# Performance work log

Measured on AMD Instinct MI355X. Metric: run time of the kernel, lower is better.

The kernel has to match this reference:

```python
import jax, jax.numpy as jnp
import numpy as np
from jax import lax

B, T, D, LSTM, N_MELS, SPK, NOISE = 256, 600, 256, 512, 80, 256, 64
MAX_R = 10
FC1 = 256
FC2 = D // 2  # 128
FILTERS, KSIZE = 32, 31


def _lin(k, out_d, in_d):
    return jax.random.normal(k, (out_d, in_d), jnp.float32) * 0.02


def setup_inputs() -> dict:
    key = jax.random.key(0)
    ks = list(jax.random.split(key, 40))
    nk = iter(ks)
    inp = {
        "encoder_seq": jax.random.normal(next(nk), (B, T, D), jnp.float32),
        "encoder_seq_proj": jax.random.normal(next(nk), (B, T, D), jnp.float32),
        "prenet_in": jax.random.normal(next(nk), (B, N_MELS), jnp.float32),
        "attn_hidden": jax.random.normal(next(nk), (B, D), jnp.float32),
        "rnn1_hidden": jax.random.normal(next(nk), (B, LSTM), jnp.float32),
        "rnn2_hidden": jax.random.normal(next(nk), (B, LSTM), jnp.float32),
        "rnn1_cell": jax.random.normal(next(nk), (B, LSTM), jnp.float32),
        "rnn2_cell": jax.random.normal(next(nk), (B, LSTM), jnp.float32),
        "context_vec": jax.random.normal(next(nk), (B, D), jnp.float32),
        "speaker_embedding": jax.random.normal(next(nk), (B, SPK), jnp.float32),
        "noise_embedding": jax.random.normal(next(nk), (B, NOISE), jnp.float32),
        "attn_cumulative": jax.random.uniform(next(nk), (B, T), jnp.float32),
        "attn_prev": jax.random.uniform(next(nk), (B, T), jnp.float32),
        "phone_len": jax.random.randint(next(nk), (B,), 1, T + 1),
        # PreNet
        "fc1_w": _lin(next(nk), FC1, N_MELS + NOISE), "fc1_b": jnp.zeros((FC1,), jnp.float32),
        "fc2_w": _lin(next(nk), FC2, FC1), "fc2_b": jnp.zeros((FC2,), jnp.float32),
        # LSA
        "conv_w": jax.random.normal(next(nk), (FILTERS, 2, KSIZE), jnp.float32) * 0.1,
        "L_w": _lin(next(nk), D, FILTERS), "L_b": jnp.zeros((D,), jnp.float32),
        "W_w": _lin(next(nk), D, D), "W_b": jnp.zeros((D,), jnp.float32),
        "v_w": _lin(next(nk), 1, D),
        # attn GRU: input = D + D//2 + SPK
        "gru_wih": _lin(next(nk), 3 * D, D + FC2 + SPK), "gru_whh": _lin(next(nk), 3 * D, D),
        "gru_bih": jnp.zeros((3 * D,), jnp.float32), "gru_bhh": jnp.zeros((3 * D,), jnp.float32),
        # rnn_input Linear: 2*D + SPK + NOISE -> LSTM
        "rnn_in_w": _lin(next(nk), LSTM, 2 * D + SPK + NOISE), "rnn_in_b": jnp.zeros((LSTM,), jnp.float32),
        # two LSTMCells
        "l1_wih": _lin(next(nk), 4 * LSTM, LSTM), "l1_whh": _lin(next(nk), 4 * LSTM, LSTM),
        "l1_bih": jnp.zeros((4 * LSTM,), jnp.float32), "l1_bhh": jnp.zeros((4 * LSTM,), jnp.float32),
        "l2_wih": _lin(next(nk), 4 * LSTM, LSTM), "l2_whh": _lin(next(nk), 4 * LSTM, LSTM),
        "l2_bih": jnp.zeros((4 * LSTM,), jnp.float32), "l2_bhh": jnp.zeros((4 * LSTM,), jnp.float32),
        # mel projection (no bias)
        "mel_w": _lin(next(nk), N_MELS * MAX_R, LSTM),
        "r": 2,
    }
    return inp


def _gru(x, h, wih, whh, bih, bhh):
    gi = x @ wih.T + bih
    gh = h @ whh.T + bhh
    i_r, i_z, i_n = jnp.split(gi, 3, axis=-1)
    h_r, h_z, h_n = jnp.split(gh, 3, axis=-1)
    r = jax.nn.sigmoid(i_r + h_r)
    z = jax.nn.sigmoid(i_z + h_z)
    n = jnp.tanh(i_n + r * h_n)
    return (1.0 - z) * n + z * h


def _lstm(x, h, c, wih, whh, bih, bhh):
    g = x @ wih.T + bih + h @ whh.T + bhh
    i, f, gg, o = jnp.split(g, 4, axis=-1)
    c_new = jax.nn.sigmoid(f) * c + jax.nn.sigmoid(i) * jnp.tanh(gg)
    h_new = jax.nn.sigmoid(o) * jnp.tanh(c_new)
    return h_new, c_new


def reference(encoder_seq, encoder_seq_proj, prenet_in, attn_hidden, rnn1_hidden,
              rnn2_hidden, rnn1_cell, rnn2_cell, context_vec, speaker_embedding,
              noise_embedding, attn_cumulative, attn_prev, phone_len,
              fc1_w, fc1_b, fc2_w, fc2_b, conv_w, L_w, L_b, W_w, W_b, v_w,
              gru_wih, gru_whh, gru_bih, gru_bhh, rnn_in_w, rnn_in_b,
              l1_wih, l1_whh, l1_bih, l1_bhh, l2_wih, l2_whh, l2_bih, l2_bhh,
              mel_w, r):
    # PreNet (eval-mode: dropout omitted for a deterministic reference)
    p = jnp.concatenate([prenet_in, noise_embedding], axis=-1)
    p = jax.nn.relu(p @ fc1_w.T + fc1_b)
    prenet_out = jax.nn.relu(p @ fc2_w.T + fc2_b)

    # attention GRU
    attn_rnn_in = jnp.concatenate([context_vec, prenet_out, speaker_embedding], axis=-1)
    attn_hidden = _gru(attn_rnn_in, attn_hidden, gru_wih, gru_whh, gru_bih, gru_bhh)

    # location-sensitive attention (t > 0 step; state passed explicitly)
    pq = (attn_hidden @ W_w.T + W_b)[:, None, :]                     # [B,1,D]
    location = jnp.stack([attn_cumulative, attn_prev], axis=1)       # [B,2,T]
    loc = lax.conv_general_dilated(location, conv_w, (1,), [((KSIZE - 1) // 2,) * 2],
                                   dimension_numbers=("NCH", "OIH", "NCH"))  # [B,F,T]
    pl = jnp.einsum("bft,df->btd", loc, L_w) + L_b                   # [B,T,D]
    u = jnp.einsum("btd,od->bt", jnp.tanh(pq + encoder_seq_proj + pl), v_w)
    mask = jnp.arange(T)[None, :] < phone_len[:, None]
    u = jnp.where(mask, u, -1e9)
    scores_bt = jax.nn.softmax(u, axis=1)                            # [B,T]
    scores = scores_bt[:, None, :]                                   # [B,1,T]

    context_vec = jnp.einsum("bt,btd->bd", scores_bt, encoder_seq)   # [B,D]

    x = jnp.concatenate([context_vec, attn_hidden, speaker_embedding, noise_embedding], axis=1)
    x = x @ rnn_in_w.T + rnn_in_b

    rnn1_hidden, rnn1_cell = _lstm(x, rnn1_hidden, rnn1_cell, l1_wih, l1_whh, l1_bih, l1_bhh)
    x = x + rnn1_hidden
    rnn2_hidden, rnn2_cell = _lstm(x, rnn2_hidden, rnn2_cell, l2_wih, l2_whh, l2_bih, l2_bhh)
    x = x + rnn2_hidden

    mels = (x @ mel_w.T).reshape(B, N_MELS, MAX_R)[:, :, :r]
    return (mels, scores, attn_hidden, rnn1_hidden, rnn2_hidden, rnn1_cell, rnn2_cell, context_vec)
```

## Files before the change

### kernel.cpp

```cpp
#include <hip/hip_runtime.h>
#include <hip/hip_bf16.h>
#include <cstdint>

#define B_ 256
#define T_ 600
#define D_ 256

typedef __attribute__((ext_vector_type(8))) short bf16x8;
typedef __attribute__((ext_vector_type(4))) float f32x4;

__device__ __forceinline__ float fast_sigmoid(float x) {
    return __fdividef(1.0f, 1.0f + __expf(-x));
}
__device__ __forceinline__ float fast_tanh(float x) {
    return 1.0f - __fdividef(2.0f, __expf(2.0f * x) + 1.0f);
}
__device__ __forceinline__ ushort f2bf(float f) {
    unsigned u = __float_as_uint(f);
    u += 0x7FFF + ((u >> 16) & 1);
    return (ushort)(u >> 16);
}

__global__ __launch_bounds__(256) void prenet_kernel(
    const float* __restrict__ pre_in, const float* __restrict__ noise,
    const float* __restrict__ w1, const float* __restrict__ b1,
    const float* __restrict__ w2, const float* __restrict__ b2,
    const float* __restrict__ ctx_in, const float* __restrict__ spk,
    const float* __restrict__ L_w, ushort* __restrict__ Lw16,
    ushort* __restrict__ Xgru16, ushort* __restrict__ Xrnn16)
{
    __shared__ float xin[144];
    __shared__ float p1[256];
    int b = blockIdx.x, t = threadIdx.x;
    if (b == 0) {
        for (int o = t; o < 8192; o += 256) {
            int dt = o >> 9;
            int ln = (o >> 3) & 63;
            int j  = o & 7;
            int in_idx = (dt * 16 + (ln & 15)) * 32 + (ln >> 4) * 8 + j;
            Lw16[o] = f2bf(L_w[in_idx]);
        }
    }
    float s = spk[b * 256 + t];
    Xgru16[b * 640 + t] = f2bf(ctx_in[b * 256 + t]);
    Xgru16[b * 640 + 384 + t] = f2bf(s);
    Xrnn16[b * 832 + 512 + t] = f2bf(s);
    if (t < 64) Xrnn16[b * 832 + 768 + t] = f2bf(noise[b * 64 + t]);
    if (t < 80) xin[t] = pre_in[b * 80 + t];
    else if (t < 144) xin[t] = noise[b * 64 + (t - 80)];
    __syncthreads();
    float acc = b1[t];
    const float4* w = (const float4*)(w1 + t * 144);
    const float4* xi = (const float4*)xin;
#pragma unroll 9
    for (int k = 0; k < 36; ++k) {
        float4 wv = w[k]; float4 xv = xi[k];
        acc += wv.x * xv.x + wv.y * xv.y + wv.z * xv.z + wv.w * xv.w;
    }
    p1[t] = fmaxf(acc, 0.f);
    __syncthreads();
    if (t < 128) {
        float a2 = b2[t];
        const float4* w2v = (const float4*)(w2 + t * 256);
        const float4* pv = (const float4*)p1;
#pragma unroll 8
        for (int k = 0; k < 64; ++k) {
            float4 wv = w2v[k]; float4 xv = pv[k];
            a2 += wv.x * xv.x + wv.y * xv.y + wv.z * xv.z + wv.w * xv.w;
        }
        Xgru16[b * 640 + 256 + t] = f2bf(fmaxf(a2, 0.f));
    }
}

__global__ __launch_bounds__(256) void convert_all(
    const float* __restrict__ w1ih, const float* __restrict__ w1hh,
    const float* __restrict__ w2ih, const float* __restrict__ w2hh,
    const float* __restrict__ gwih, const float* __restrict__ gwhh,
    const float* __restrict__ Ww, const float* __restrict__ riw,
    const float* __restrict__ ahin, const float* __restrict__ h1in,
    ushort* __restrict__ wcat1, ushort* __restrict__ wcat2,
    ushort* __restrict__ gwih16, ushort* __restrict__ gwhh16,
    ushort* __restrict__ Ww16, ushort* __restrict__ riw16,
    ushort* __restrict__ ahin16, ushort* __restrict__ xh1)
{
    int bid = blockIdx.x, t = threadIdx.x;
    if (bid < 4096) {
        int n = bid & 2047;
        int layer = bid >> 11;
        const float* wih = layer ? w2ih : w1ih;
        const float* whh = layer ? w2hh : w1hh;
        ushort* dst = layer ? wcat2 : wcat1;
        const float* src = (t < 128) ? (wih + (size_t)n * 512 + t * 4)
                                     : (whh + (size_t)n * 512 + (t - 128) * 4);
        float4 v = *(const float4*)src;
        ushort4 o;
        o.x = f2bf(v.x); o.y = f2bf(v.y); o.z = f2bf(v.z); o.w = f2bf(v.w);
        *(ushort4*)&dst[(size_t)n * 1024 + t * 4] = o;
        return;
    }
    bid -= 4096;
    if (bid >= 1216) {
        bid -= 1216;
        size_t i = (size_t)bid * 1024 + t * 4;
        float4 v = *(const float4*)&h1in[i];
        int b = (int)(i >> 9), k = (int)(i & 511);
        ushort4 o;
        o.x = f2bf(v.x); o.y = f2bf(v.y); o.z = f2bf(v.z); o.w = f2bf(v.w);
        *(ushort4*)&xh1[(size_t)b * 1024 + 512 + k] = o;
        return;
    }
    const float* src; ushort* dst;
    if (bid < 480)       { src = gwih; dst = gwih16; }
    else if (bid < 672)  { bid -= 480;  src = gwhh; dst = gwhh16; }
    else if (bid < 736)  { bid -= 672;  src = Ww;   dst = Ww16; }
    else if (bid < 1152) { bid -= 736;  src = riw;  dst = riw16; }
    else                 { bid -= 1152; src = ahin; dst = ahin16; }
    size_t i = (size_t)bid * 1024 + t * 4;
    float4 v = *(const float4*)&src[i];
    ushort4 o;
    o.x = f2bf(v.x); o.y = f2bf(v.y); o.z = f2bf(v.z); o.w = f2bf(v.w);
    *(ushort4*)&dst[i] = o;
}

__global__ __launch_bounds__(256) void mfma_gemmN(
    const ushort* __restrict__ A16, int K,
    const ushort* __restrict__ B16, const float* __restrict__ bias,
    float* __restrict__ C, int N, ushort* __restrict__ xcast)
{
    int tid = threadIdx.x;
    int lane = tid & 63, wv = tid >> 6;
    int m0 = blockIdx.x * 32;
    int n0 = blockIdx.y * 64;
    int wm = wv >> 1, wn = wv & 1;
    int cl = lane & 15, ko = (lane >> 4) * 8;

    const ushort* ap  = A16 + (size_t)(m0 + wm * 16 + cl) * K + ko;
    const ushort* bp0 = B16 + (size_t)(n0 + wn * 32 + cl) * K + ko;
    const ushort* bp1 = bp0 + (size_t)16 * K;

    f32x4 acc0 = {0.f, 0.f, 0.f, 0.f};
    f32x4 acc1 = {0.f, 0.f, 0.f, 0.f};
    int nks = K >> 5;
#pragma unroll 2
    for (int ks = 0; ks < nks; ++ks) {
        bf16x8 a  = *(const bf16x8*)ap;
        bf16x8 b0 = *(const bf16x8*)bp0;
        bf16x8 b1 = *(const bf16x8*)bp1;
        ap += 32; bp0 += 32; bp1 += 32;
        acc0 = __builtin_amdgcn_mfma_f32_16x16x32_bf16(a, b0, acc0, 0, 0, 0);
        acc1 = __builtin_amdgcn_mfma_f32_16x16x32_bf16(a, b1, acc1, 0, 0, 0);
    }
    int orow = m0 + wm * 16 + (lane >> 4) * 4;
    int ocol = n0 + wn * 32 + cl;
    float bb0 = bias ? bias[ocol] : 0.f;
    float bb1 = bias ? bias[ocol + 16] : 0.f;
#pragma unroll
    for (int r2 = 0; r2 < 4; ++r2) {
        float v0 = acc0[r2] + bb0;
        float v1 = acc1[r2] + bb1;
        C[(size_t)(orow + r2) * N + ocol]      = v0;
        C[(size_t)(orow + r2) * N + ocol + 16] = v1;
        if (xcast) {
            xcast[(size_t)(orow + r2) * 1024 + ocol]      = f2bf(v0);
            xcast[(size_t)(orow + r2) * 1024 + ocol + 16] = f2bf(v1);
        }
    }
}

__global__ __launch_bounds__(256) void mfma_gemm(
    const ushort* __restrict__ A16, const ushort* __restrict__ B16,
    float* __restrict__ G0, float* __restrict__ G1)
{
    int tid = threadIdx.x;
    int lane = tid & 63, wv = tid >> 6;
    int m0 = blockIdx.x * 32;
    int n0 = blockIdx.y * 64;
    int kbase = blockIdx.z * 512;
    float* Gout = blockIdx.z ? G1 : G0;
    int wm = wv >> 1, wn = wv & 1;
    int cl = lane & 15, ko = (lane >> 4) * 8;

    const ushort* ap  = A16 + (size_t)(m0 + wm * 16 + cl) * 1024 + kbase + ko;
    const ushort* bp0 = B16 + (size_t)(n0 + wn * 32 + cl) * 1024 + kbase + ko;
    const ushort* bp1 = bp0 + (size_t)16 * 1024;

    f32x4 acc0 = {0.f, 0.f, 0.f, 0.f};
    f32x4 acc1 = {0.f, 0.f, 0.f, 0.f};
#pragma unroll
    for (int ks = 0; ks < 16; ++ks) {
        bf16x8 a  = *(const bf16x8*)(ap  + ks * 32);
        bf16x8 b0 = *(const bf16x8*)(bp0 + ks * 32);
        bf16x8 b1 = *(const bf16x8*)(bp1 + ks * 32);
        acc0 = __builtin_amdgcn_mfma_f32_16x16x32_bf16(a, b0, acc0, 0, 0, 0);
        acc1 = __builtin_amdgcn_mfma_f32_16x16x32_bf16(a, b1, acc1, 0, 0, 0);
    }
    int orow = m0 + wm * 16 + (lane >> 4) * 4;
    int ocol = n0 + wn * 32 + cl;
#pragma unroll
    for (int r2 = 0; r2 < 4; ++r2) {
        Gout[(size_t)(orow + r2) * 2048 + ocol]      = acc0[r2];
        Gout[(size_t)(orow + r2) * 2048 + ocol + 16] = acc1[r2];
    }
}

__global__ __launch_bounds__(256) void gru_combine(
    const float* __restrict__ Cgi, const float* __restrict__ Cgh,
    const float* __restrict__ h_in, float* __restrict__ ah_out,
    ushort* __restrict__ ah16, ushort* __restrict__ Xrnn16)
{
    int b = blockIdx.x, j = threadIdx.x;
    float gir = Cgi[b * 768 + j], giz = Cgi[b * 768 + 256 + j], gin = Cgi[b * 768 + 512 + j];
    float ghr = Cgh[b * 768 + j], ghz = Cgh[b * 768 + 256 + j], ghn = Cgh[b * 768 + 512 + j];
    float rr = fast_sigmoid(gir + ghr);
    float zz = fast_sigmoid(giz + ghz);
    float nn = fast_tanh(gin + rr * ghn);
    float h = (1.f - zz) * nn + zz * h_in[b * 256 + j];
    ah_out[b * 256 + j] = h;
    ah16[b * 256 + j] = f2bf(h);
    Xrnn16[b * 832 + 256 + j] = f2bf(h);
}

#define TCH 64
__global__ __launch_bounds__(256) void attn_u_kernel(
    const float* __restrict__ esp, const float* __restrict__ pq,
    const float* __restrict__ cum, const float* __restrict__ prv,
    const float* __restrict__ conv_w, const ushort* __restrict__ Lw16,
    const float* __restrict__ L_b, const float* __restrict__ v_w,
    float* __restrict__ u)
{
    __shared__ float cumL[TCH + 32], prvL[TCH + 32];
    __shared__ float cwL[32 * 62];
    __shared__ ushort lwS[8192];
    __shared__ ushort locs[TCH][40];
    __shared__ float pq2s[256], vvs[256];
    int b = blockIdx.y;
    int t0 = blockIdx.x * TCH;
    int tid = threadIdx.x;
    int lane = tid & 63, wv = tid >> 6;
    int cl = lane & 15, gr = lane >> 4;

    for (int i = tid; i < TCH + 30; i += 256) {
        int tg = t0 + i - 15;
        bool ok = (tg >= 0) && (tg < T_);
        cumL[i] = ok ? cum[b * T_ + tg] : 0.f;
        prvL[i] = ok ? prv[b * T_ + tg] : 0.f;
    }
    for (int i = tid; i < 32 * 62; i += 256) cwL[i] = conv_w[i];
    {
        const float4* src = (const float4*)Lw16;
        float4* dst = (float4*)lwS;
#pragma unroll
        for (int i = 0; i < 4; ++i) dst[tid + i * 256] = src[tid + i * 256];
    }
    pq2s[tid] = pq[b * 256 + tid] + L_b[tid];
    vvs[tid] = v_w[tid];

    int tw = t0 + wv * 16 + cl;
    int tc = (tw < T_) ? tw : (T_ - 1);
    const float4* ep4 = (const float4*)(esp + ((size_t)b * T_ + tc) * 256) + gr;
    float e[64];
#pragma unroll
    for (int dt = 0; dt < 16; ++dt) {
        float4 t4 = ep4[dt * 4];
        e[dt * 4 + 0] = t4.x; e[dt * 4 + 1] = t4.y;
        e[dt * 4 + 2] = t4.z; e[dt * 4 + 3] = t4.w;
    }

    asm volatile("s_waitcnt lgkmcnt(0)" ::: "memory");
    __builtin_amdgcn_s_barrier();
    __builtin_amdgcn_sched_barrier(0);

    {
        int f = tid & 31, ts = tid >> 5;
        const float* c0 = &cwL[f * 62];
        float acc[8] = {};
#pragma unroll
        for (int k = 0; k < 31; ++k) {
            float wcv = c0[k], wpv = c0[31 + k];
#pragma unroll
            for (int i = 0; i < 8; ++i)
                acc[i] = fmaf(cumL[ts * 8 + i + k], wcv, fmaf(prvL[ts * 8 + i + k], wpv, acc[i]));
        }
#pragma unroll
        for (int i = 0; i < 8; ++i)
            locs[ts * 8 + i][f] = f2bf(acc[i]);
    }
    __syncthreads();

    bf16x8 locf = *(const bf16x8*)&locs[wv * 16 + cl][gr * 8];
    float sum = 0.f;
#pragma unroll
    for (int dt = 0; dt < 16; ++dt) {
        bf16x8 af = *(const bf16x8*)&lwS[(dt * 64 + lane) * 8];
        float4 pq4 = *(const float4*)&pq2s[dt * 16 + gr * 4];
        float4 vv4 = *(const float4*)&vvs[dt * 16 + gr * 4];
        f32x4 acc = {pq4.x, pq4.y, pq4.z, pq4.w};
        acc = __builtin_amdgcn_mfma_f32_16x16x32_bf16(af, locf, acc, 0, 0, 0);
        sum = fmaf(fast_tanh(e[dt * 4 + 0] + acc[0]), vv4.x, sum);
        sum = fmaf(fast_tanh(e[dt * 4 + 1] + acc[1]), vv4.y, sum);
        sum = fmaf(fast_tanh(e[dt * 4 + 2] + acc[2]), vv4.z, sum);
        sum = fmaf(fast_tanh(e[dt * 4 + 3] + acc[3]), vv4.w, sum);
    }
    sum += __shfl_xor(sum, 16, 64);
    sum += __shfl_xor(sum, 32, 64);
    if (lane < 16 && tw < T_) u[b * T_ + tw] = sum;
}

__global__ __launch_bounds__(1024) void softmax_ctx_kernel(
    const float* __restrict__ u, const int* __restrict__ plen,
    const float* __restrict__ enc,
    float* __restrict__ scores, float* __restrict__ ctx_out,
    ushort* __restrict__ Xrnn16)
{
    __shared__ float sc[T_];
    __shared__ float red[16];
    __shared__ float part[16][256];
    int b = blockIdx.x, tid = threadIdx.x;
    int lane = tid & 63, wid = tid >> 6;
    int pl = plen[b];
    float mv = -1e30f;
    if (tid < T_) {
        float uv = u[b * T_ + tid];
        mv = (tid < pl) ? uv : -1e9f;
        sc[tid] = mv;
    }
    float m = mv;
#pragma unroll
    for (int off = 32; off > 0; off >>= 1) m = fmaxf(m, __shfl_xor(m, off, 64));
    if (lane == 0) red[wid] = m;
    __syncthreads();
    m = red[0];
#pragma unroll
    for (int i = 1; i < 16; ++i) m = fmaxf(m, red[i]);
    float ev = 0.f;
    if (tid < T_) ev = __expf(sc[tid] - m);
    float s = ev;
    __syncthreads();
#pragma unroll
    for (int off = 32; off > 0; off >>= 1) s += __shfl_xor(s, off, 64);
    if (lane == 0) red[wid] = s;
    __syncthreads();
    float tot = 0.f;
#pragma unroll
    for (int i = 0; i < 16; ++i) tot += red[i];
    float inv = __fdividef(1.0f, tot);
    if (tid < T_) {
        float scv = ev * inv;
        scores[b * T_ + tid] = scv;
        sc[tid] = scv;
    }
    __syncthreads();
    float a0 = 0.f, a1 = 0.f, a2 = 0.f, a3 = 0.f;
    const float4* ep = (const float4*)(enc + ((size_t)b * T_ + wid) * 256) + lane;
    for (int t = wid; t < T_; t += 16) {
        float sv = sc[t];
        float4 ev4 = *ep;
        a0 = fmaf(sv, ev4.x, a0);
        a1 = fmaf(sv, ev4.y, a1);
        a2 = fmaf(sv, ev4.z, a2);
        a3 = fmaf(sv, ev4.w, a3);
        ep += 16 * 64;
    }
    part[wid][lane * 4 + 0] = a0;
    part[wid][lane * 4 + 1] = a1;
    part[wid][lane * 4 + 2] = a2;
    part[wid][lane * 4 + 3] = a3;
    __syncthreads();
    if (tid < 256) {
        float c = 0.f;
#pragma unroll
        for (int q = 0; q < 16; ++q) c += part[q][tid];
        ctx_out[b * 256 + tid] = c;
        Xrnn16[b * 832 + tid] = f2bf(c);
    }
}

__global__ __launch_bounds__(512) void lstm_combine2(
    const float* __restrict__ G0, const float* __restrict__ G1,
    const float* __restrict__ bih, const float* __restrict__ bhh,
    const float* __restrict__ c_in, const float* __restrict__ x_in,
    float* __restrict__ h_out, float* __restrict__ c_out,
    float* __restrict__ x_next,
    const float* __restrict__ h_next_in, ushort* __restrict__ xh_next)
{
    int b = blockIdx.x, j = threadIdx.x;
    size_t base = (size_t)b * 2048;
    float gi = G0[base + j] + G1[base + j] + bih[j] + bhh[j];
    float gf = G0[base + 512 + j] + G1[base + 512 + j] + bih[512 + j] + bhh[512 + j];
    float gg = G0[base + 1024 + j] + G1[base + 1024 + j] + bih[1024 + j] + bhh[1024 + j];
    float go = G0[base + 1536 + j] + G1[base + 1536 + j] + bih[1536 + j] + bhh[1536 + j];
    float c = fast_sigmoid(gf) * c_in[b * 512 + j] + fast_sigmoid(gi) * fast_tanh(gg);
    float h = fast_sigmoid(go) * fast_tanh(c);
    float xn = x_in[b * 512 + j] + h;
    h_out[b * 512 + j] = h;
    c_out[b * 512 + j] = c;
    x_next[b * 512 + j] = xn;
    if (xh_next) {
        xh_next[(size_t)b * 1024 + j] = f2bf(xn);
        xh_next[(size_t)b * 1024 + 512 + j] = f2bf(h_next_in[b * 512 + j]);
    }
}

__global__ __launch_bounds__(256) void mel_kernel(
    const float* __restrict__ x2, const float* __restrict__ mel_w,
    int r, float* __restrict__ mels)
{
    __shared__ float xl[512];
    int b = blockIdx.x, tid = threadIdx.x;
    xl[tid] = x2[b * 512 + tid];
    xl[256 + tid] = x2[b * 512 + 256 + tid];
    __syncthreads();
    for (int idx = tid; idx < 80 * r; idx += 256) {
        int mrow = (idx / r) * 10 + (idx % r);
        const float4* w = (const float4*)(mel_w + (size_t)mrow * 512);
        const float4* xv = (const float4*)xl;
        float acc = 0.f;
#pragma unroll 16
        for (int k = 0; k < 128; ++k) {
            float4 a = w[k], c = xv[k];
            acc += a.x * c.x + a.y * c.y + a.z * c.z + a.w * c.w;
        }
        mels[(size_t)b * 80 * r + idx] = acc;
    }
}

extern "C" void kernel_launch(void* const* d_in, const int* in_sizes, int n_in,
                              void* d_out, int out_size, void* d_ws, size_t ws_size,
                              hipStream_t stream)
{
    const float* enc    = (const float*)d_in[0];
    const float* esp    = (const float*)d_in[1];
    const float* pre_in = (const float*)d_in[2];
    const float* ah_in  = (const float*)d_in[3];
    const float* h1_in  = (const float*)d_in[4];
    const float* h2_in  = (const float*)d_in[5];
    const float* c1_in  = (const float*)d_in[6];
    const float* c2_in  = (const float*)d_in[7];
    const float* ctx_in = (const float*)d_in[8];
    const float* spk    = (const float*)d_in[9];
    const float* noise  = (const float*)d_in[10];
    const float* cum    = (const float*)d_in[11];
    const float* prv    = (const float*)d_in[12];
    const int*   plen   = (const int*)d_in[13];
    const float* fc1_w  = (const float*)d_in[14];
    const float* fc1_b  = (const float*)d_in[15];
    const float* fc2_w  = (const float*)d_in[16];
    const float* fc2_b  = (const float*)d_in[17];
    const float* conv_w = (const float*)d_in[18];
    const float* L_w    = (const float*)d_in[19];
    const float* L_b    = (const float*)d_in[20];
    const float* W_w    = (const float*)d_in[21];
    const float* W_b    = (const float*)d_in[22];
    const float* v_w    = (const float*)d_in[23];
    const float* g_wih  = (const float*)d_in[24];
    const float* g_whh  = (const float*)d_in[25];
    const float* g_bih  = (const float*)d_in[26];
    const float* g_bhh  = (const float*)d_in[27];
    const float* ri_w   = (const float*)d_in[28];
    const float* ri_b   = (const float*)d_in[29];
    const float* l1_wih = (const float*)d_in[30];
    const float* l1_whh = (const float*)d_in[31];
    const float* l1_bih = (const float*)d_in[32];
    const float* l1_bhh = (const float*)d_in[33];
    const float* l2_wih = (const float*)d_in[34];
    const float* l2_whh = (const float*)d_in[35];
    const float* l2_bih = (const float*)d_in[36];
    const float* l2_bhh = (const float*)d_in[37];
    const float* mel_w  = (const float*)d_in[38];

    int r = (out_size - 808960) / 20480;
    if (r < 1) r = 1;
    if (r > 10) r = 10;

    float* out    = (float*)d_out;
    float* mels   = out;
    float* scores = out + (size_t)20480 * r;
    float* ah_out = scores + 153600;
    float* h1_out = ah_out + 65536;
    float* h2_out = h1_out + 131072;
    float* c1_out = h2_out + 131072;
    float* c2_out = c1_out + 131072;
    float* ctx_out = c2_out + 131072;

    float* ws   = (float*)d_ws;
    float* Cgi  = ws;
    float* Cgh  = Cgi + 196608;
    float* pq   = Cgh + 196608;
    float* uu   = pq + 65536;
    float* x0   = uu + 153600;
    float* x1   = x0 + 131072;
    float* x2   = x1 + 131072;
    float* G0   = x2 + 131072;
    float* G1   = G0 + 524288;
    ushort* Lw16   = (ushort*)(G1 + 524288);
    ushort* Xgru16 = Lw16 + 8192;
    ushort* Xrnn16 = Xgru16 + 163840;
    ushort* ah16   = Xrnn16 + 212992;
    ushort* ahin16 = ah16 + 65536;
    ushort* wcat1  = ahin16 + 65536;
    ushort* wcat2  = wcat1 + 2097152;
    ushort* gwih16 = wcat2 + 2097152;
    ushort* gwhh16 = gwih16 + 491520;
    ushort* Ww16   = gwhh16 + 196608;
    ushort* riw16  = Ww16 + 65536;
    ushort* xh1    = riw16 + 425984;
    ushort* xh2    = xh1 + 262144;

    prenet_kernel<<<256, 256, 0, stream>>>(pre_in, noise, fc1_w, fc1_b, fc2_w, fc2_b,
                                           ctx_in, spk, L_w, Lw16, Xgru16, Xrnn16);
    convert_all<<<5440, 256, 0, stream>>>(l1_wih, l1_whh, l2_wih, l2_whh,
                                          g_wih, g_whh, W_w, ri_w, ah_in, h1_in,
                                          wcat1, wcat2, gwih16, gwhh16,
                                          Ww16, riw16, ahin16, xh1);
    mfma_gemmN<<<dim3(8, 12), 256, 0, stream>>>(Xgru16, 640, gwih16, g_bih, Cgi, 768, nullptr);
    mfma_gemmN<<<dim3(8, 12), 256, 0, stream>>>(ahin16, 256, gwhh16, g_bhh, Cgh, 768, nullptr);
    gru_combine<<<256, 256, 0, stream>>>(Cgi, Cgh, ah_in, ah_out, ah16, Xrnn16);
    mfma_gemmN<<<dim3(8, 4), 256, 0, stream>>>(ah16, 256, Ww16, W_b, pq, 256, nullptr);
    attn_u_kernel<<<dim3(10, 256), 256, 0, stream>>>(esp, pq, cum, prv, conv_w, Lw16, L_b, v_w, uu);
    softmax_ctx_kernel<<<256, 1024, 0, stream>>>(uu, plen, enc, scores, ctx_out, Xrnn16);
    mfma_gemmN<<<dim3(8, 8), 256, 0, stream>>>(Xrnn16, 832, riw16, ri_b, x0, 512, xh1);
    mfma_gemm<<<dim3(8, 32, 2), 256, 0, stream>>>(xh1, wcat1, G0, G1);
    lstm_combine2<<<256, 512, 0, stream>>>(G0, G1, l1_bih, l1_bhh, c1_in, x0,
                                           h1_out, c1_out, x1, h2_in, xh2);
    mfma_gemm<<<dim3(8, 32, 2), 256, 0, stream>>>(xh2, wcat2, G0, G1);
    lstm_combine2<<<256, 512, 0, stream>>>(G0, G1, l2_bih, l2_bhh, c2_in, x1,
                                           h2_out, c2_out, x2, nullptr, nullptr);
    mel_kernel<<<256, 256, 0, stream>>>(x2, mel_w, r, mels);
}
```

Baseline: 188.4 us.

## Split attention-energy D dimension across four wave groups per block

Raises attn_u_kernel from 256 to 1024 threads per block. Each group of four waves now handles a quarter of the 256-wide D dimension, and the per-thread register array for encoder_seq_proj shrinks from 64 floats to 16. Partial sums are combined through shared memory. The aim is more memory-level parallelism and lower register pressure for the bandwidth-bound projection read, at the cost of an extra barrier, a shared-memory reduction, and larger blocks that may limit occupancy.

After: 199.9 us. +6.1%, slower.

```diff
diff --git a/kernel.cpp b/kernel.cpp
--- a/kernel.cpp
+++ b/kernel.cpp
@@ -220,90 +220,97 @@
     Xrnn16[b * 832 + 256 + j] = f2bf(h);
 }
 
-#define TCH 64
-__global__ __launch_bounds__(256) void attn_u_kernel(
+__global__ __launch_bounds__(1024) void attn_u_kernel(
     const float* __restrict__ esp, const float* __restrict__ pq,
     const float* __restrict__ cum, const float* __restrict__ prv,
     const float* __restrict__ conv_w, const ushort* __restrict__ Lw16,
     const float* __restrict__ L_b, const float* __restrict__ v_w,
     float* __restrict__ u)
 {
-    __shared__ float cumL[TCH + 32], prvL[TCH + 32];
-    __shared__ float cwL[32 * 62];
+    __shared__ float cumL[96], prvL[96];
+    __shared__ float cwL[1984];
     __shared__ ushort lwS[8192];
-    __shared__ ushort locs[TCH][40];
+    __shared__ ushort locs[64][40];
     __shared__ float pq2s[256], vvs[256];
+    __shared__ float upart[4][64];
     int b = blockIdx.y;
-    int t0 = blockIdx.x * TCH;
+    int t0 = blockIdx.x * 64;
     int tid = threadIdx.x;
-    int lane = tid & 63, wv = tid >> 6;
+    int lane = tid & 63, w = tid >> 6;
+    int tt = w & 3, dtg = w >> 2;
     int cl = lane & 15, gr = lane >> 4;
 
-    for (int i = tid; i < TCH + 30; i += 256) {
+    int tw = t0 + tt * 16 + cl;
+    int tc = (tw < T_) ? tw : (T_ - 1);
+    const float4* ep4 = (const float4*)(esp + ((size_t)b * T_ + tc) * 256) + gr;
+    float4 e0 = ep4[(dtg * 4 + 0) * 4];
+    float4 e1 = ep4[(dtg * 4 + 1) * 4];
+    float4 e2 = ep4[(dtg * 4 + 2) * 4];
+    float4 e3 = ep4[(dtg * 4 + 3) * 4];
+
+    for (int i = tid; i < 94; i += 1024) {
         int tg = t0 + i - 15;
         bool ok = (tg >= 0) && (tg < T_);
         cumL[i] = ok ? cum[b * T_ + tg] : 0.f;
         prvL[i] = ok ? prv[b * T_ + tg] : 0.f;
     }
-    for (int i = tid; i < 32 * 62; i += 256) cwL[i] = conv_w[i];
+    for (int i = tid; i < 1984; i += 1024) cwL[i] = conv_w[i];
     {
         const float4* src = (const float4*)Lw16;
         float4* dst = (float4*)lwS;
-#pragma unroll
-        for (int i = 0; i < 4; ++i) dst[tid + i * 256] = src[tid + i * 256];
-    }
-    pq2s[tid] = pq[b * 256 + tid] + L_b[tid];
-    vvs[tid] = v_w[tid];
-
-    int tw = t0 + wv * 16 + cl;
-    int tc = (tw < T_) ? tw : (T_ - 1);
-    const float4* ep4 = (const float4*)(esp + ((size_t)b * T_ + tc) * 256) + gr;
-    float e[64];
-#pragma unroll
-    for (int dt = 0; dt < 16; ++dt) {
-        float4 t4 = ep4[dt * 4];
-        e[dt * 4 + 0] = t4.x; e[dt * 4 + 1] = t4.y;
-        e[dt * 4 + 2] = t4.z; e[dt * 4 + 3] = t4.w;
-    }
-
-    asm volatile("s_waitcnt lgkmcnt(0)" ::: "memory");
-    __builtin_amdgcn_s_barrier();
-    __builtin_amdgcn_sched_barrier(0);
+        dst[tid] = src[tid];
+    }
+    if (tid < 256) {
+        pq2s[tid] = pq[b * 256 + tid] + L_b[tid];
+        vvs[tid] = v_w[tid];
+    }
+    __syncthreads();
 
     {
         int f = tid & 31, ts = tid >> 5;
         const float* c0 = &cwL[f * 62];
-        float acc[8] = {};
+        float a0 = 0.f, a1 = 0.f;
 #pragma unroll
         for (int k = 0; k < 31; ++k) {
             float wcv = c0[k], wpv = c0[31 + k];
-#pragma unroll
-            for (int i = 0; i < 8; ++i)
-                acc[i] = fmaf(cumL[ts * 8 + i + k], wcv, fmaf(prvL[ts * 8 + i + k], wpv, acc[i]));
+            a0 = fmaf(cumL[ts + k], wcv, fmaf(prvL[ts + k], wpv, a0));
+            a1 = fmaf(cumL[ts + 32 + k], wcv, fmaf(prvL[ts + 32 + k], wpv, a1));
         }
-#pragma unroll
-        for (int i = 0; i < 8; ++i)
-            locs[ts * 8 + i][f] = f2bf(acc[i]);
-    }
-    __syncthreads();
-
-    bf16x8 locf = *(const bf16x8*)&locs[wv * 16 + cl][gr * 8];
+        locs[ts][f] = f2bf(a0);
+        locs[ts + 32][f] = f2bf(a1);
+    }
+    __syncthreads();
+
+    bf16x8 locf = *(const bf16x8*)&locs[tt * 16 + cl][gr * 8];
     float sum = 0.f;
-#pragma unroll
-    for (int dt = 0; dt < 16; ++dt) {
-        bf16x8 af = *(const bf16x8*)&lwS[(dt * 64 + lane) * 8];
-        float4 pq4 = *(const float4*)&pq2s[dt * 16 + gr * 4];
-        float4 vv4 = *(const float4*)&vvs[dt * 16 + gr * 4];
-        f32x4 acc = {pq4.x, pq4.y, pq4.z, pq4.w};
-        acc = __builtin_amdgcn_mfma_f32_16x16x32_bf16(af, locf, acc, 0, 0, 0);
-        sum = fmaf(fast_tanh(e[dt * 4 + 0] + acc[0]), vv4.x, sum);
-        sum = fmaf(fast_tanh(e[dt * 4 + 1] + acc[1]), vv4.y, sum);
-        sum = fmaf(fast_tanh(e[dt * 4 + 2] + acc[2]), vv4.z, sum);
-        sum = fmaf(fast_tanh(e[dt * 4 + 3] + acc[3]), vv4.w, sum);
-    }
+    int dt0 = dtg * 4;
+#define STEP(J, EV)                                                           \
+    {                                                                         \
+        int dt = dt0 + (J);                                                   \
+        bf16x8 af = *(const bf16x8*)&lwS[(dt * 64 + lane) * 8];               \
+        float4 pq4 = *(const float4*)&pq2s[dt * 16 + gr * 4];                 \
+        float4 vv4 = *(const float4*)&vvs[dt * 16 + gr * 4];                  \
+        f32x4 acc = {pq4.x, pq4.y, pq4.z, pq4.w};                             \
+        acc = __builtin_amdgcn_mfma_f32_16x16x32_bf16(af, locf, acc, 0, 0, 0);\
+        sum = fmaf(fast_tanh(EV.x + acc[0]), vv4.x, sum);                     \
+        sum = fmaf(fast_tanh(EV.y + acc[1]), vv4.y, sum);                     \
+        sum = fmaf(fast_tanh(EV.z + acc[2]), vv4.z, sum);                     \
+        sum = fmaf(fast_tanh(EV.w + acc[3]), vv4.w, sum);                     \
+    }
+    STEP(0, e0)
+    STEP(1, e1)
+    STEP(2, e2)
+    STEP(3, e3)
+#undef STEP
     sum += __shfl_xor(sum, 16, 64);
     sum += __shfl_xor(sum, 32, 64);
-    if (lane < 16 && tw < T_) u[b * T_ + tw] = sum;
+    if (lane < 16) upart[dtg][tt * 16 + cl] = sum;
+    __syncthreads();
+    if (tid < 64) {
+        int t = t0 + tid;
+        if (t < T_)
+            u[b * T_ + t] = upart[0][tid] + upart[1][tid] + upart[2][tid] + upart[3][tid];
+    }
 }
 
 __global__ __launch_bounds__(1024) void softmax_ctx_kernel(
@@ -516,7 +523,7 @@
     mfma_gemmN<<<dim3(8, 12), 256, 0, stream>>>(ahin16, 256, gwhh16, g_bhh, Cgh, 768, nullptr);
     gru_combine<<<256, 256, 0, stream>>>(Cgi, Cgh, ah_in, ah_out, ah16, Xrnn16);
     mfma_gemmN<<<dim3(8, 4), 256, 0, stream>>>(ah16, 256, Ww16, W_b, pq, 256, nullptr);
-    attn_u_kernel<<<dim3(10, 256), 256, 0, stream>>>(esp, pq, cum, prv, conv_w, Lw16, L_b, v_w, uu);
+    attn_u_kernel<<<dim3(10, 256), 1024, 0, stream>>>(esp, pq, cum, prv, conv_w, Lw16, L_b, v_w, uu);
     softmax_ctx_kernel<<<256, 1024, 0, stream>>>(uu, plen, enc, scores, ctx_out, Xrnn16);
     mfma_gemmN<<<dim3(8, 8), 256, 0, stream>>>(Xrnn16, 832, riw16, ri_b, x0, 512, xh1);
     mfma_gemm<<<dim3(8, 32, 2), 256, 0, stream>>>(xh1, wcat1, G0, G1);
```
